# Optimization experiments

Measured on AMD Instinct MI355X. Metric: run time of the kernel, lower is better.

The kernel has to match this reference:

```python
import jax, jax.numpy as jnp
import numpy as np

B, T_IN, D = 16, 512, 256
MAX_DUR = 16


def setup_inputs() -> dict:
    key = jax.random.key(0)
    k1, k2 = jax.random.split(key)
    duration = jax.random.randint(k1, (B, T_IN), 0, MAX_DUR, dtype=jnp.int32)
    encoder_outputs = jax.random.normal(k2, (B, T_IN, D), dtype=jnp.float32)
    mask = jnp.ones((B, T_IN), dtype=bool)
    return {"encoder_outputs": encoder_outputs, "duration": duration, "mask": mask}


def reference(encoder_outputs, duration, mask):
    # duration is a concrete int array here, so T_out is a static Python int
    t_max = int(jnp.max(jnp.sum(duration, axis=-1)))
    d = duration.astype(jnp.float32)
    # frame centers per token: c[b, i] = cumsum(d)[b, i] - 0.5 * d[b, i]
    c = (jnp.cumsum(d, axis=-1) - 0.5 * d)[:, :, None]          # [B, T_in, 1]
    t = jnp.arange(1, t_max + 1, dtype=jnp.float32)[None, None, :]  # [1, 1, T_out]
    w1 = jnp.exp(-0.1 * (t - c) ** 2)                           # [B, T_in, T_out]
    w2 = jnp.sum(w1, axis=1, keepdims=True)                     # [B, 1, T_out]
    w2 = jnp.where(w2 == 0.0, 1.0, w2)
    w = w1 / w2                                                 # [B, T_in, T_out]
    # out[b, t, d] = sum_i w[b, i, t] * enc[b, i, d]
    out = jnp.einsum('bit,bid->btd', w, encoder_outputs)        # [B, T_out, D]
    return (out, w)
```

## Files before the change

### kernel.cpp

```cpp
#include <hip/hip_runtime.h>

#define B_    16
#define T_IN  512
#define D_    256
#define TM    64
#define KI    32
#define AP    40

typedef __attribute__((ext_vector_type(8))) short short8;
typedef __attribute__((ext_vector_type(4))) float f32x4;

__device__ __forceinline__ unsigned short f2bf(float x) {
    unsigned u = __builtin_bit_cast(unsigned, x);
    u += 0x7fff + ((u >> 16) & 1);
    return (unsigned short)(u >> 16);
}

__global__ __launch_bounds__(256, 3) void fused_kernel(
    const float* __restrict__ enc,
    const int*   __restrict__ dur,
    float* __restrict__ out,
    float* __restrict__ wout,
    int t_out)
{
    __shared__ int   sd[T_IN];
    __shared__ float sc[T_IN];
    __shared__ float red[4][TM];
    __shared__ float sinv[TM];
    __shared__ __align__(16) unsigned short A_lds[TM * AP];

    const int tid = threadIdx.x;
    const int b   = blockIdx.y;
    const int t0  = blockIdx.x * TM;

    const int v0 = dur[b * T_IN + tid];
    const int v1 = dur[b * T_IN + tid + 256];
    sd[tid] = v0;
    sd[tid + 256] = v1;
    __syncthreads();
    for (int off = 1; off < T_IN; off <<= 1) {
        const int a0 = (tid >= off) ? sd[tid - off] : 0;
        const int a1 = sd[tid + 256 - off];
        __syncthreads();
        sd[tid] += a0;
        sd[tid + 256] += a1;
        __syncthreads();
    }
    sc[tid]       = (float)sd[tid]       - 0.5f * (float)v0;
    sc[tid + 256] = (float)sd[tid + 256] - 0.5f * (float)v1;
    __syncthreads();

    const int tq = tid & 63;
    const int qq = tid >> 6;
    const float tv = (float)(t0 + tq + 1);

    {
        float s = 0.f;
        const int i0 = qq * 128;
        for (int i = 0; i < 128; ++i) {
            const float d = tv - sc[i0 + i];
            s += __expf(-0.1f * d * d);
        }
        red[qq][tq] = s;
        __syncthreads();
        if (qq == 0) {
            const float w2 = red[0][tq] + red[1][tq] + red[2][tq] + red[3][tq];
            sinv[tq] = (w2 == 0.f) ? 1.f : 1.f / w2;
        }
        __syncthreads();
    }
    const float inv_t = sinv[tq];
    const bool  t_ok  = (t0 + tq) < t_out;

    const int lane  = tid & 63;
    const int wave  = tid >> 6;
    const int mrow  = lane & 15;
    const int quad  = lane >> 4;
    const int dbase = wave * 64;
    const int iq0   = qq * 8;

    f32x4 acc[4][4];
    #pragma unroll
    for (int mf = 0; mf < 4; ++mf)
        #pragma unroll
        for (int nf = 0; nf < 4; ++nf)
            acc[mf][nf] = (f32x4){0.f, 0.f, 0.f, 0.f};

    const float* encB = enc + (long long)b * T_IN * D_;
    float* wB = wout + (long long)b * T_IN * t_out + (t0 + tq);

    for (int kc = 0; kc < T_IN; kc += KI) {
        __syncthreads();

        {
            unsigned short tmp[8];
            #pragma unroll
            for (int j = 0; j < 8; ++j) {
                const float d = tv - sc[kc + iq0 + j];
                const float e = __expf(-0.1f * d * d);
                tmp[j] = f2bf(e);
                if (t_ok) wB[(long long)(kc + iq0 + j) * t_out] = e * inv_t;
            }
            *(short8*)&A_lds[tq * AP + iq0] = *(const short8*)tmp;
        }
        __syncthreads();

        short8 av[4];
        #pragma unroll
        for (int mf = 0; mf < 4; ++mf)
            av[mf] = *(const short8*)&A_lds[(mf * 16 + mrow) * AP + quad * 8];

        #pragma unroll
        for (int nf = 0; nf < 4; ++nf) {
            const float* p = encB + (long long)(kc + quad * 8) * D_ + dbase + nf * 16 + mrow;
            unsigned short bt[8];
            #pragma unroll
            for (int j = 0; j < 8; ++j) bt[j] = f2bf(p[j * D_]);
            const short8 bv = *(const short8*)bt;
            #pragma unroll
            for (int mf = 0; mf < 4; ++mf)
                acc[mf][nf] = __builtin_amdgcn_mfma_f32_16x16x32_bf16(av[mf], bv, acc[mf][nf], 0, 0, 0);
        }
    }

    #pragma unroll
    for (int mf = 0; mf < 4; ++mf) {
        #pragma unroll
        for (int r = 0; r < 4; ++r) {
            const int tl = mf * 16 + quad * 4 + r;
            const int t  = t0 + tl;
            if (t < t_out) {
                const float inv = sinv[tl];
                #pragma unroll
                for (int nf = 0; nf < 4; ++nf)
                    out[((long long)b * t_out + t) * D_ + dbase + nf * 16 + mrow] = acc[mf][nf][r] * inv;
            }
        }
    }
}

extern "C" void kernel_launch(void* const* d_in, const int* in_sizes, int n_in,
                              void* d_out, int out_size, void* d_ws, size_t ws_size,
                              hipStream_t stream) {
    const float* enc = (const float*)d_in[0];
    const int*   dur = (const int*)d_in[1];

    const int t_out = out_size / (B_ * (D_ + T_IN));

    float* out  = (float*)d_out;
    float* wout = (float*)d_out + (size_t)B_ * t_out * D_;

    dim3 grid((t_out + TM - 1) / TM, B_);
    fused_kernel<<<grid, 256, 0, stream>>>(enc, dur, out, wout, t_out);
}
```

Baseline: 260.9 us.

## Pre-transpose encoder to bf16 and split weight writes into a separate kernel

Adds a transpose kernel that converts the encoder outputs to bf16 in a [B, D, T_in] layout. This lets the MFMA kernel load B fragments as contiguous 16-byte vectors instead of eight strided fp32 loads with per-element conversion. The large normalised weight tensor is now written by its own kernel using nontemporal stores, leaving the matmul kernel free of those scattered writes. The A tile is double buffered in LDS, which removes one barrier per K step. In exchange, the prefix scan and normaliser are computed twice, and the bf16 scratch buffer lives in the tail of the weight output region before that region is overwritten.

Measured after the change: 278.2 us. +6.6%, slower.

```diff
diff --git a/kernel.cpp b/kernel.cpp
--- a/kernel.cpp
+++ b/kernel.cpp
@@ -16,18 +16,46 @@
     return (unsigned short)(u >> 16);
 }
 
-__global__ __launch_bounds__(256, 3) void fused_kernel(
-    const float* __restrict__ enc,
+__global__ __launch_bounds__(256) void transpose_kernel(
+    const float* __restrict__ enc, unsigned short* __restrict__ encT)
+{
+    __shared__ float tile[64][65];
+    const int tid = threadIdx.x;
+    const int b  = blockIdx.z;
+    const int i0 = blockIdx.x * 64;
+    const int d0 = blockIdx.y * 64;
+    #pragma unroll
+    for (int p = 0; p < 4; ++p) {
+        const int idx = p * 256 + tid;
+        const int r   = idx >> 4;
+        const int c4  = (idx & 15) * 4;
+        const float4 v = *(const float4*)&enc[((long long)b * T_IN + i0 + r) * D_ + d0 + c4];
+        tile[r][c4 + 0] = v.x; tile[r][c4 + 1] = v.y;
+        tile[r][c4 + 2] = v.z; tile[r][c4 + 3] = v.w;
+    }
+    __syncthreads();
+    #pragma unroll
+    for (int p = 0; p < 8; ++p) {
+        const int idx = p * 256 + tid;
+        const int dr = idx >> 5;
+        const int ip = idx & 31;
+        const unsigned pk = (unsigned)f2bf(tile[2 * ip][dr])
+                          | ((unsigned)f2bf(tile[2 * ip + 1][dr]) << 16);
+        *(unsigned*)&encT[((long long)b * D_ + d0 + dr) * T_IN + i0 + ip * 2] = pk;
+    }
+}
+
+__global__ __launch_bounds__(256, 4) void mfma_kernel(
+    const unsigned short* __restrict__ encT,
     const int*   __restrict__ dur,
     float* __restrict__ out,
-    float* __restrict__ wout,
     int t_out)
 {
     __shared__ int   sd[T_IN];
     __shared__ float sc[T_IN];
     __shared__ float red[4][TM];
     __shared__ float sinv[TM];
-    __shared__ __align__(16) unsigned short A_lds[TM * AP];
+    __shared__ __align__(16) unsigned short A_lds[2][TM * AP];
 
     const int tid = threadIdx.x;
     const int b   = blockIdx.y;
@@ -35,15 +63,13 @@
 
     const int v0 = dur[b * T_IN + tid];
     const int v1 = dur[b * T_IN + tid + 256];
-    sd[tid] = v0;
-    sd[tid + 256] = v1;
+    sd[tid] = v0; sd[tid + 256] = v1;
     __syncthreads();
     for (int off = 1; off < T_IN; off <<= 1) {
         const int a0 = (tid >= off) ? sd[tid - off] : 0;
         const int a1 = sd[tid + 256 - off];
         __syncthreads();
-        sd[tid] += a0;
-        sd[tid + 256] += a1;
+        sd[tid] += a0; sd[tid + 256] += a1;
         __syncthreads();
     }
     sc[tid]       = (float)sd[tid]       - 0.5f * (float)v0;
@@ -69,14 +95,11 @@
         }
         __syncthreads();
     }
-    const float inv_t = sinv[tq];
-    const bool  t_ok  = (t0 + tq) < t_out;
 
     const int lane  = tid & 63;
-    const int wave  = tid >> 6;
     const int mrow  = lane & 15;
     const int quad  = lane >> 4;
-    const int dbase = wave * 64;
+    const int dbase = qq * 64;
     const int iq0   = qq * 8;
 
     f32x4 acc[4][4];
@@ -86,37 +109,30 @@
         for (int nf = 0; nf < 4; ++nf)
             acc[mf][nf] = (f32x4){0.f, 0.f, 0.f, 0.f};
 
-    const float* encB = enc + (long long)b * T_IN * D_;
-    float* wB = wout + (long long)b * T_IN * t_out + (t0 + tq);
-
-    for (int kc = 0; kc < T_IN; kc += KI) {
-        __syncthreads();
-
+    const unsigned short* encTb = encT + (long long)b * D_ * T_IN;
+
+    for (int ib = 0; ib < T_IN / KI; ++ib) {
+        const int kc = ib * KI;
+        unsigned short* Ab = A_lds[ib & 1];
         {
             unsigned short tmp[8];
             #pragma unroll
             for (int j = 0; j < 8; ++j) {
                 const float d = tv - sc[kc + iq0 + j];
-                const float e = __expf(-0.1f * d * d);
-                tmp[j] = f2bf(e);
-                if (t_ok) wB[(long long)(kc + iq0 + j) * t_out] = e * inv_t;
+                tmp[j] = f2bf(__expf(-0.1f * d * d));
             }
-            *(short8*)&A_lds[tq * AP + iq0] = *(const short8*)tmp;
+            *(short8*)&Ab[tq * AP + iq0] = *(const short8*)tmp;
         }
         __syncthreads();
 
         short8 av[4];
         #pragma unroll
         for (int mf = 0; mf < 4; ++mf)
-            av[mf] = *(const short8*)&A_lds[(mf * 16 + mrow) * AP + quad * 8];
+            av[mf] = *(const short8*)&Ab[(mf * 16 + mrow) * AP + quad * 8];
 
         #pragma unroll
         for (int nf = 0; nf < 4; ++nf) {
-            const float* p = encB + (long long)(kc + quad * 8) * D_ + dbase + nf * 16 + mrow;
-            unsigned short bt[8];
-            #pragma unroll
-            for (int j = 0; j < 8; ++j) bt[j] = f2bf(p[j * D_]);
-            const short8 bv = *(const short8*)bt;
+            const short8 bv = *(const short8*)&encTb[(long long)(dbase + nf * 16 + mrow) * T_IN + kc + quad * 8];
             #pragma unroll
             for (int mf = 0; mf < 4; ++mf)
                 acc[mf][nf] = __builtin_amdgcn_mfma_f32_16x16x32_bf16(av[mf], bv, acc[mf][nf], 0, 0, 0);
@@ -133,8 +149,71 @@
                 const float inv = sinv[tl];
                 #pragma unroll
                 for (int nf = 0; nf < 4; ++nf)
-                    out[((long long)b * t_out + t) * D_ + dbase + nf * 16 + mrow] = acc[mf][nf][r] * inv;
+                    __builtin_nontemporal_store(acc[mf][nf][r] * inv,
+                        &out[((long long)b * t_out + t) * D_ + dbase + nf * 16 + mrow]);
             }
+        }
+    }
+}
+
+__global__ __launch_bounds__(256, 4) void wwrite_kernel(
+    const int* __restrict__ dur, float* __restrict__ wout, int t_out)
+{
+    __shared__ int   sd[T_IN];
+    __shared__ float sc[T_IN];
+    __shared__ float red[4][TM];
+    __shared__ float sinv[TM];
+
+    const int tid = threadIdx.x;
+    const int b   = blockIdx.y;
+    const int t0  = blockIdx.x * TM;
+
+    const int v0 = dur[b * T_IN + tid];
+    const int v1 = dur[b * T_IN + tid + 256];
+    sd[tid] = v0; sd[tid + 256] = v1;
+    __syncthreads();
+    for (int off = 1; off < T_IN; off <<= 1) {
+        const int a0 = (tid >= off) ? sd[tid - off] : 0;
+        const int a1 = sd[tid + 256 - off];
+        __syncthreads();
+        sd[tid] += a0; sd[tid + 256] += a1;
+        __syncthreads();
+    }
+    sc[tid]       = (float)sd[tid]       - 0.5f * (float)v0;
+    sc[tid + 256] = (float)sd[tid + 256] - 0.5f * (float)v1;
+    __syncthreads();
+
+    const int tq = tid & 63;
+    const int qq = tid >> 6;
+    const float tv = (float)(t0 + tq + 1);
+
+    {
+        float s = 0.f;
+        const int i0 = qq * 128;
+        for (int i = 0; i < 128; ++i) {
+            const float d = tv - sc[i0 + i];
+            s += __expf(-0.1f * d * d);
+        }
+        red[qq][tq] = s;
+        __syncthreads();
+        if (qq == 0) {
+            const float w2 = red[0][tq] + red[1][tq] + red[2][tq] + red[3][tq];
+            sinv[tq] = (w2 == 0.f) ? 1.f : 1.f / w2;
+        }
+        __syncthreads();
+    }
+
+    if (t0 + tq >= t_out) return;
+    const float inv = sinv[tq];
+    float* wB = wout + (long long)b * T_IN * t_out + (t0 + tq);
+
+    for (int kc = 0; kc < T_IN; kc += KI) {
+        #pragma unroll
+        for (int j = 0; j < 8; ++j) {
+            const int i = kc + qq * 8 + j;
+            const float d = tv - sc[i];
+            __builtin_nontemporal_store(__expf(-0.1f * d * d) * inv,
+                                        &wB[(long long)i * t_out]);
         }
     }
 }
@@ -149,7 +228,12 @@
 
     float* out  = (float*)d_out;
     float* wout = (float*)d_out + (size_t)B_ * t_out * D_;
+    unsigned short* encT =
+        (unsigned short*)(wout + (size_t)B_ * T_IN * t_out) - (size_t)B_ * D_ * T_IN;
+
+    transpose_kernel<<<dim3(T_IN / 64, D_ / 64, B_), 256, 0, stream>>>(enc, encT);
 
     dim3 grid((t_out + TM - 1) / TM, B_);
-    fused_kernel<<<grid, 256, 0, stream>>>(enc, dur, out, wout, t_out);
-}
+    mfma_kernel<<<grid, 256, 0, stream>>>(encT, dur, out, t_out);
+    wwrite_kernel<<<grid, 256, 0, stream>>>(dur, wout, t_out);
+}
```
